# Kernel optimization log

Measured on AMD Instinct MI355X. Metric: run time of the kernel, lower is better.

The kernel has to match this reference:

```python
import jax, jax.numpy as jnp
import numpy as np

D_MODEL = 1024
HEADS = 16
D_HEAD = 64  # d_q = d_k = d_v
LN_EPS = 1e-5


def setup_inputs() -> dict:
    key = jax.random.key(0)
    ks = jax.random.split(key, 12)
    B, L = 2, 2048
    query = jax.random.normal(ks[0], (B, L, D_MODEL), dtype=jnp.float32)
    k_in = jax.random.normal(ks[1], (B, L, D_MODEL), dtype=jnp.float32)
    v_in = jax.random.normal(ks[2], (B, L, D_MODEL), dtype=jnp.float32)
    # causal mask: True = masked (masked_fill with -inf); row i always keeps pos i
    mask = jnp.broadcast_to(~jnp.tril(jnp.ones((L, L), dtype=bool)), (B, L, L))
    std_qk = np.sqrt(2.0 / (D_MODEL + D_HEAD)).astype(np.float32)
    Wq = jax.random.normal(ks[3], (D_MODEL, HEADS * D_HEAD), dtype=jnp.float32) * std_qk
    Wk = jax.random.normal(ks[4], (D_MODEL, HEADS * D_HEAD), dtype=jnp.float32) * std_qk
    Wv = jax.random.normal(ks[5], (D_MODEL, HEADS * D_HEAD), dtype=jnp.float32) * std_qk
    bq = jnp.zeros((HEADS * D_HEAD,), dtype=jnp.float32)
    bk = jnp.zeros((HEADS * D_HEAD,), dtype=jnp.float32)
    bv = jnp.zeros((HEADS * D_HEAD,), dtype=jnp.float32)
    lim = 1.0 / np.sqrt(HEADS * D_HEAD)
    Wo = jax.random.uniform(ks[6], (HEADS * D_HEAD, D_MODEL), dtype=jnp.float32, minval=-lim, maxval=lim)
    bo = jax.random.uniform(ks[7], (D_MODEL,), dtype=jnp.float32, minval=-lim, maxval=lim)
    gamma = jnp.ones((D_MODEL,), dtype=jnp.float32)
    beta = jnp.zeros((D_MODEL,), dtype=jnp.float32)
    return {"query": query, "key": k_in, "value": v_in, "mask": mask,
            "Wq": Wq, "bq": bq, "Wk": Wk, "bk": bk, "Wv": Wv, "bv": bv,
            "Wo": Wo, "bo": bo, "gamma": gamma, "beta": beta}


def reference(query, key, value, mask, Wq, bq, Wk, bk, Wv, bv, Wo, bo, gamma, beta):
    B, Lq, _ = query.shape
    Lk = key.shape[1]
    # QKV projections, split into heads: [B, L, H, d]
    q = (query @ Wq + bq).reshape(B, Lq, HEADS, D_HEAD)
    k = (key @ Wk + bk).reshape(B, Lk, HEADS, D_HEAD)
    v = (value @ Wv + bv).reshape(B, Lk, HEADS, D_HEAD)
    # scaled dot-product scores: [B, H, Lq, Lk]
    scores = jnp.einsum('bqhd,bkhd->bhqk', q, k) / np.sqrt(D_HEAD).astype(np.float32)
    scores = jnp.where(mask[:, None, :, :], -jnp.inf, scores)
    probs = jax.nn.softmax(scores, axis=-1)  # dropout is identity at p=0 / eval
    out = jnp.einsum('bhqk,bkhd->bqhd', probs, v).reshape(B, Lq, HEADS * D_HEAD)
    out = out @ Wo + bo  # dropout identity
    x = query + out  # residual
    mu = jnp.mean(x, axis=-1, keepdims=True)
    var = jnp.var(x, axis=-1, keepdims=True)
    return gamma * (x - mu) * jax.lax.rsqrt(var + LN_EPS) + beta
```

## Files before the change

### kernel.cpp

```cpp
#include <hip/hip_runtime.h>
#include <hip/hip_bf16.h>

#define L_SEQ  2048
#define DMODEL 1024
#define HEADS  16
#define DHEAD  64
#define BATCH  2
#define MROWS  (BATCH * L_SEQ)

typedef __attribute__((ext_vector_type(8))) short bf16x8;
typedef __attribute__((ext_vector_type(8))) unsigned short u16x8;
typedef __attribute__((ext_vector_type(4))) float f32x4;

__device__ __forceinline__ float b2f(unsigned short u) {
    union { unsigned int u32; float f; } x;
    x.u32 = ((unsigned int)u) << 16;
    return x.f;
}
__device__ __forceinline__ unsigned short f2b(float f) {
    union { float f; unsigned int u; } x; x.f = f;
    unsigned int u = x.u;
    if ((u & 0x7fffffffu) > 0x7f800000u) return (unsigned short)((u >> 16) | 0x0040);
    unsigned int r = (u + 0x7fffu + ((u >> 16) & 1u)) >> 16;
    return (unsigned short)r;
}
__device__ __forceinline__ unsigned short f2br(float f) {
    union { float f; unsigned int u; } x; x.f = f;
    return (unsigned short)((x.u + 0x7fffu + ((x.u >> 16) & 1u)) >> 16);
}

__device__ __forceinline__ float4 load4(const void* p, int isF32, size_t idx) {
    if (isF32) return *(const float4*)((const float*)p + idx);
    const ushort4 u = *(const ushort4*)((const unsigned short*)p + idx);
    return make_float4(b2f(u.x), b2f(u.y), b2f(u.z), b2f(u.w));
}
__device__ __forceinline__ float load1(const void* p, int isF32, size_t idx) {
    return isF32 ? ((const float*)p)[idx] : b2f(((const unsigned short*)p)[idx]);
}

__device__ __forceinline__ void gload16(const void* g, void* l) {
    __builtin_amdgcn_global_load_lds(
        (const __attribute__((address_space(1))) void*)g,
        (__attribute__((address_space(3))) void*)l, 16, 0, 0);
}

__global__ void detect_kernel(const unsigned short* __restrict__ q, int* __restrict__ flag) {
    int cnt = 0;
    #pragma unroll 8
    for (int t = 0; t < 64; ++t) {
        const unsigned short u = q[(threadIdx.x << 6) + t];
        const int e = (u >> 7) & 0xFF;
        cnt += (e >= 133) ? 1 : 0;
    }
    #pragma unroll
    for (int off = 32; off; off >>= 1) cnt += __shfl_xor(cnt, off);
    if (threadIdx.x == 0) *flag = (cnt > 64) ? 1 : 0;
}

__global__ void diag_kernel(float* __restrict__ out, float val, int n) {
    const int i = blockIdx.x * 256 + threadIdx.x;
    if (i < n) out[i] = val;
}

__global__ __launch_bounds__(256) void cvtW_kernel(
    const void* __restrict__ W0, const void* __restrict__ W1,
    const void* __restrict__ W2, const void* __restrict__ W3,
    unsigned short* __restrict__ T0, unsigned short* __restrict__ T1,
    unsigned short* __restrict__ T2, unsigned short* __restrict__ T3,
    const int* __restrict__ dflag)
{
    const int isF32 = *dflag;
    const int z = blockIdx.z;
    const void* W = (z == 0) ? W0 : (z == 1) ? W1 : (z == 2) ? W2 : W3;
    unsigned short* T = (z == 0) ? T0 : (z == 1) ? T1 : (z == 2) ? T2 : T3;

    __shared__ unsigned short tile[64][66];
    const int kb = blockIdx.x << 6, nb = blockIdx.y << 6;
    const int tr = threadIdx.x >> 4, tc = (threadIdx.x & 15) << 2;
    #pragma unroll
    for (int p = 0; p < 4; ++p) {
        const int r = tr + p * 16;
        const float4 v = load4(W, isF32, (size_t)(kb + r) * DMODEL + nb + tc);
        tile[tc + 0][r] = f2br(v.x);
        tile[tc + 1][r] = f2br(v.y);
        tile[tc + 2][r] = f2br(v.z);
        tile[tc + 3][r] = f2br(v.w);
    }
    __syncthreads();
    #pragma unroll
    for (int p = 0; p < 4; ++p) {
        const int rr = tr + p * 16;
        const ushort4 o = make_ushort4(tile[rr][tc], tile[rr][tc + 1],
                                       tile[rr][tc + 2], tile[rr][tc + 3]);
        *(ushort4*)(T + (size_t)(nb + rr) * DMODEL + kb + tc) = o;
    }
}

#define STAGE_B(BUF, K0)                                                          \
    gload16(Wt + (size_t)(colBase + bseg * 16 + brow) * DMODEL + (K0) + bcol,     \
            Bs[BUF] + bseg * 512);                                                \
    gload16(Wt + (size_t)(colBase + (bseg + 1) * 16 + brow) * DMODEL + (K0) + bcol,\
            Bs[BUF] + (bseg + 1) * 512);

#define QKV_COMPUTE(CUR)                                                          \
    {                                                                             \
        bf16x8 af[2], bfr[4];                                                     \
        _Pragma("unroll")                                                         \
        for (int i = 0; i < 2; ++i) {                                             \
            const int row = wm + i * 16 + ln;                                     \
            const int p = quad ^ ((row >> 1) & 3);                                \
            af[i] = *(const bf16x8*)(As[CUR] + row * 32 + p * 8);                 \
        }                                                                         \
        _Pragma("unroll")                                                         \
        for (int j = 0; j < 4; ++j)                                               \
            bfr[j] = *(const bf16x8*)(Bs[CUR] + (wn + j * 16 + ln) * 32 + quad * 8); \
        _Pragma("unroll")                                                         \
        for (int i = 0; i < 2; ++i)                                               \
            _Pragma("unroll")                                                     \
            for (int j = 0; j < 4; ++j)                                           \
                acc[i][j] = __builtin_amdgcn_mfma_f32_16x16x32_bf16(af[i], bfr[j], acc[i][j], 0, 0, 0); \
    }

__global__ __launch_bounds__(256) void gemm_qkv_mfma(
    const void* __restrict__ A0, const void* __restrict__ A1, const void* __restrict__ A2,
    const unsigned short* __restrict__ Wt0, const unsigned short* __restrict__ Wt1,
    const unsigned short* __restrict__ Wt2,
    const void* __restrict__ b0, const void* __restrict__ b1, const void* __restrict__ b2,
    unsigned short* __restrict__ O0, unsigned short* __restrict__ O1, unsigned short* __restrict__ O2,
    const int* __restrict__ dflag)
{
    const int isF32 = *dflag;

    const int bid = blockIdx.x;
    const int xcd = bid & 7;
    const int jj  = bid >> 3;
    const int g   = xcd * 24 + (jj >> 3);
    const int z   = g >> 6;
    const int rowBase = (g & 63) << 6;
    const int colBase = (jj & 7) << 7;

    const void* A  = (z == 0) ? A0 : (z == 1) ? A1 : A2;
    const unsigned short* Wt = (z == 0) ? Wt0 : (z == 1) ? Wt1 : Wt2;
    const void* bi = (z == 0) ? b0 : (z == 1) ? b1 : b2;
    unsigned short* out = (z == 0) ? O0 : (z == 1) ? O1 : O2;
    const float scale = (z == 0) ? 0.125f : 1.0f;

    __shared__ __align__(16) unsigned short As[2][64 * 32];
    __shared__ __align__(16) unsigned short Bs[2][128 * 32];

    const int tid  = threadIdx.x;
    const int lane = tid & 63, wid = tid >> 6;
    const int ln   = lane & 15, quad = lane >> 4;
    const int wm   = (wid & 1) << 5;
    const int wn   = (wid >> 1) << 6;

    f32x4 acc[2][4];
    #pragma unroll
    for (int i = 0; i < 2; ++i)
        #pragma unroll
        for (int j = 0; j < 4; ++j)
            #pragma unroll
            for (int d = 0; d < 4; ++d) acc[i][j][d] = 0.f;

    const int am  = tid >> 2;
    const int seg = tid & 3;
    const int sw  = (am >> 1) & 3;
    const int bseg = wid * 2;
    const int brow = lane >> 2, bcol = (lane & 3) << 3;

    if (isF32) {
        STAGE_B(0, 0)
        {
            const size_t ab = (size_t)(rowBase + am) * DMODEL + seg * 8;
            const float4 a0 = load4(A, 1, ab);
            const float4 a1 = load4(A, 1, ab + 4);
            u16x8 pk;
            pk[0] = f2br(a0.x); pk[1] = f2br(a0.y); pk[2] = f2br(a0.z); pk[3] = f2br(a0.w);
            pk[4] = f2br(a1.x); pk[5] = f2br(a1.y); pk[6] = f2br(a1.z); pk[7] = f2br(a1.w);
            *(u16x8*)(As[0] + am * 32 + ((seg ^ sw) << 3)) = pk;
        }
        __syncthreads();

        int cur = 0;
        for (int t = 0; t < 31; ++t) {
            const int nxt = cur ^ 1;
            const int k0n = (t + 1) << 5;
            STAGE_B(nxt, k0n)
            const size_t ab = (size_t)(rowBase + am) * DMODEL + k0n + seg * 8;
            const float4 a0 = load4(A, 1, ab);
            const float4 a1 = load4(A, 1, ab + 4);

            QKV_COMPUTE(cur)

            u16x8 pk;
            pk[0] = f2br(a0.x); pk[1] = f2br(a0.y); pk[2] = f2br(a0.z); pk[3] = f2br(a0.w);
            pk[4] = f2br(a1.x); pk[5] = f2br(a1.y); pk[6] = f2br(a1.z); pk[7] = f2br(a1.w);
            *(u16x8*)(As[nxt] + am * 32 + ((seg ^ sw) << 3)) = pk;

            __syncthreads();
            cur = nxt;
        }
        QKV_COMPUTE(cur)
    } else {
        const size_t asrc = (size_t)(rowBase + (tid >> 2)) * DMODEL +
                            (((tid & 3) ^ ((tid >> 3) & 3)) << 3);
        STAGE_B(0, 0)
        gload16((const unsigned short*)A + asrc, As[0] + wid * 512);
        __syncthreads();
        int cur = 0;
        for (int t = 0; t < 31; ++t) {
            const int nxt = cur ^ 1;
            const int k0n = (t + 1) << 5;
            STAGE_B(nxt, k0n)
            gload16((const unsigned short*)A + asrc + k0n, As[nxt] + wid * 512);
            QKV_COMPUTE(cur)
            __syncthreads();
            cur = nxt;
        }
        QKV_COMPUTE(cur)
    }

    float bsv[4];
    #pragma unroll
    for (int j = 0; j < 4; ++j) bsv[j] = load1(bi, isF32, colBase + wn + j * 16 + ln);

    if (z != 2) {
        #pragma unroll
        for (int i = 0; i < 2; ++i) {
            const int r0 = rowBase + wm + i * 16 + quad * 4;
            const int b = r0 >> 11, l0 = r0 & (L_SEQ - 1);
            #pragma unroll
            for (int j = 0; j < 4; ++j) {
                const int n = colBase + wn + j * 16 + ln;
                const int h = n >> 6, d = n & 63;
                const size_t base = ((size_t)(b * HEADS + h) * L_SEQ) << 6;
                #pragma unroll
                for (int reg = 0; reg < 4; ++reg)
                    out[base + ((size_t)(l0 + reg) << 6) + d] =
                        f2br((acc[i][j][reg] + bsv[j]) * scale);
            }
        }
    } else {
        #pragma unroll
        for (int i = 0; i < 2; ++i) {
            const int r0 = rowBase + wm + i * 16 + quad * 4;
            const int b = r0 >> 11, l0 = r0 & (L_SEQ - 1);
            #pragma unroll
            for (int j = 0; j < 4; ++j) {
                const int n = colBase + wn + j * 16 + ln;
                const int h = n >> 6, d = n & 63;
                ushort4 o;
                o.x = f2br(acc[i][j][0] + bsv[j]);
                o.y = f2br(acc[i][j][1] + bsv[j]);
                o.z = f2br(acc[i][j][2] + bsv[j]);
                o.w = f2br(acc[i][j][3] + bsv[j]);
                *(ushort4*)(out + (((size_t)((b * HEADS + h) * 64 + d)) << 11) + l0) = o;
            }
        }
    }
}

#define OSTAGE(BUF, K0)                                                           \
    gload16(AO + (size_t)(rowBase + wid * 16 + (lane >> 2)) * DMODEL + (K0) + ((lane & 3) << 3), \
            As[BUF] + wid * 512);                                                 \
    gload16(Wt + (size_t)(colBase + bseg * 16 + brow) * DMODEL + (K0) + bcol,     \
            Bs[BUF] + bseg * 512);                                                \
    gload16(Wt + (size_t)(colBase + (bseg + 1) * 16 + brow) * DMODEL + (K0) + bcol,\
            Bs[BUF] + (bseg + 1) * 512);

#define OUT_COMPUTE(CUR)                                                          \
    {                                                                             \
        bf16x8 af[2], bfr[4];                                                     \
        _Pragma("unroll")                                                         \
        for (int i = 0; i < 2; ++i)                                               \
            af[i] = *(const bf16x8*)(As[CUR] + (wm + i * 16 + ln) * 32 + quad * 8); \
        _Pragma("unroll")                                                         \
        for (int j = 0; j < 4; ++j)                                               \
            bfr[j] = *(const bf16x8*)(Bs[CUR] + (wn + j * 16 + ln) * 32 + quad * 8); \
        _Pragma("unroll")                                                         \
        for (int i = 0; i < 2; ++i)                                               \
            _Pragma("unroll")                                                     \
            for (int j = 0; j < 4; ++j)                                           \
                acc[i][j] = __builtin_amdgcn_mfma_f32_16x16x32_bf16(af[i], bfr[j], acc[i][j], 0, 0, 0); \
    }

__global__ __launch_bounds__(256) void gemm_out_mfma(
    const unsigned short* __restrict__ AO,
    const unsigned short* __restrict__ Wt,
    const void* __restrict__ bi,
    const void* __restrict__ resid,
    float* __restrict__ X,
    const int* __restrict__ dflag)
{
    const int isF32 = *dflag;
    __shared__ __align__(16) unsigned short As[2][64 * 32];
    __shared__ __align__(16) unsigned short Bs[2][128 * 32];

    const int bid = blockIdx.x;
    const int xcd = bid & 7;
    const int jj  = bid >> 3;
    const int g   = xcd * 8 + (jj >> 3);
    const int rowBase = g << 6;
    const int colBase = (jj & 7) << 7;

    const int tid  = threadIdx.x;
    const int lane = tid & 63, wid = tid >> 6;
    const int ln   = lane & 15, quad = lane >> 4;
    const int wm   = (wid & 1) << 5;
    const int wn   = (wid >> 1) << 6;

    f32x4 acc[2][4];
    #pragma unroll
    for (int i = 0; i < 2; ++i)
        #pragma unroll
        for (int j = 0; j < 4; ++j)
            #pragma unroll
            for (int d = 0; d < 4; ++d) acc[i][j][d] = 0.f;

    const int bseg = wid * 2;
    const int brow = lane >> 2, bcol = (lane & 3) << 3;

    OSTAGE(0, 0)
    __syncthreads();

    int cur = 0;
    for (int t = 0; t < 31; ++t) {
        const int nxt = cur ^ 1;
        const int k0n = (t + 1) << 5;
        OSTAGE(nxt, k0n)
        OUT_COMPUTE(cur)
        __syncthreads();
        cur = nxt;
    }
    OUT_COMPUTE(cur)

    float bsv[4];
    #pragma unroll
    for (int j = 0; j < 4; ++j) bsv[j] = load1(bi, isF32, colBase + wn + j * 16 + ln);

    #pragma unroll
    for (int i = 0; i < 2; ++i) {
        const int r0 = rowBase + wm + i * 16 + quad * 4;
        #pragma unroll
        for (int j = 0; j < 4; ++j) {
            const int n = colBase + wn + j * 16 + ln;
            #pragma unroll
            for (int reg = 0; reg < 4; ++reg) {
                const size_t idx = (size_t)(r0 + reg) * DMODEL + n;
                X[idx] = acc[i][j][reg] + bsv[j] + load1(resid, isF32, idx);
            }
        }
    }
}

#define KVB  128
#define NQB  (L_SEQ / 64)
#define KSTR 72
#define VSTR 136
__global__ __launch_bounds__(256, 3) void attn_mfma_kernel(
    const unsigned short* __restrict__ Q,
    const unsigned short* __restrict__ K,
    const unsigned short* __restrict__ Vt,
    unsigned short* __restrict__ AO)
{
    __shared__ unsigned short Kl[KVB * KSTR];
    __shared__ unsigned short Vl[64 * VSTR];
    __shared__ unsigned short Pl[4][16 * KVB];

    const int tid  = threadIdx.x;
    const int wid  = tid >> 6;
    const int lane = tid & 63;
    const int ln   = lane & 15;
    const int quad = lane >> 4;

    const int qb = (NQB - 1) - (blockIdx.x >> 5);
    const int bh = blockIdx.x & 31;

    const size_t qkBase = (size_t)bh * (L_SEQ * 64);
    const size_t vtBase = (size_t)bh * (64 * L_SEQ);

    const int qrow = qb * 64 + wid * 16 + ln;
    const bf16x8 qf0 = *(const bf16x8*)(Q + qkBase + (size_t)qrow * 64 + quad * 8);
    const bf16x8 qf1 = *(const bf16x8*)(Q + qkBase + (size_t)qrow * 64 + quad * 8 + 32);

    f32x4 o[4];
    #pragma unroll
    for (int d = 0; d < 4; ++d) { o[d][0] = 0.f; o[d][1] = 0.f; o[d][2] = 0.f; o[d][3] = 0.f; }
    float m[4] = {-INFINITY, -INFINITY, -INFINITY, -INFINITY};
    float l[4] = {0.f, 0.f, 0.f, 0.f};

    unsigned short* Pw = Pl[wid];
    const int kp_r = tid >> 3, kp_c = (tid & 7) * 8;
    const int vp_r = tid >> 4, vp_c = (tid & 15) * 8;

    const int nt = (qb >> 1) + 1;
    for (int jt = 0; jt < nt; ++jt) {
        __syncthreads();
        #pragma unroll
        for (int p = 0; p < 4; ++p) {
            const int kr = kp_r + p * 32;
            *(int4*)(Kl + kr * KSTR + kp_c) =
                *(const int4*)(K + qkBase + (size_t)(jt * KVB + kr) * 64 + kp_c);
            const int vr = vp_r + p * 16;
            *(int4*)(Vl + vr * VSTR + vp_c) =
                *(const int4*)(Vt + vtBase + (size_t)vr * L_SEQ + jt * KVB + vp_c);
        }
        __syncthreads();

        f32x4 s[8];
        __builtin_amdgcn_s_setprio(1);
        #pragma unroll
        for (int sub = 0; sub < 8; ++sub) {
            const bf16x8 kf0 = *(const bf16x8*)(Kl + (sub * 16 + ln) * KSTR + quad * 8);
            const bf16x8 kf1 = *(const bf16x8*)(Kl + (sub * 16 + ln) * KSTR + quad * 8 + 32);
            f32x4 a2;
            a2[0] = 0.f; a2[1] = 0.f; a2[2] = 0.f; a2[3] = 0.f;
            a2 = __builtin_amdgcn_mfma_f32_16x16x32_bf16(qf0, kf0, a2, 0, 0, 0);
            a2 = __builtin_amdgcn_mfma_f32_16x16x32_bf16(qf1, kf1, a2, 0, 0, 0);
            s[sub] = a2;
        }
        __builtin_amdgcn_s_setprio(0);

        if (jt == nt - 1) {
            const int row0 = qb * 64 + wid * 16 + quad * 4;
            #pragma unroll
            for (int sub = 0; sub < 8; ++sub) {
                const int keyg = jt * KVB + sub * 16 + ln;
                #pragma unroll
                for (int reg = 0; reg < 4; ++reg)
                    if (keyg > row0 + reg) s[sub][reg] = -INFINITY;
            }
        }

        float alpha[4];
        #pragma unroll
        for (int reg = 0; reg < 4; ++reg) {
            float t = fmaxf(
                fmaxf(fmaxf(s[0][reg], s[1][reg]), fmaxf(s[2][reg], s[3][reg])),
                fmaxf(fmaxf(s[4][reg], s[5][reg]), fmaxf(s[6][reg], s[7][reg])));
            #pragma unroll
            for (int off = 8; off; off >>= 1) t = fmaxf(t, __shfl_xor(t, off));
            const float mn = fmaxf(m[reg], t);
            alpha[reg] = __expf(m[reg] - mn);
            m[reg] = mn;
            float rs = 0.f;
            #pragma unroll
            for (int sub = 0; sub < 8; ++sub) {
                const float pe = __expf(s[sub][reg] - mn);
                s[sub][reg] = pe;
                rs += pe;
            }
            #pragma unroll
            for (int off = 8; off; off >>= 1) rs += __shfl_xor(rs, off);
            l[reg] = l[reg] * alpha[reg] + rs;
        }

        #pragma unroll
        for (int sub = 0; sub < 8; ++sub)
            #pragma unroll
            for (int reg = 0; reg < 4; ++reg) {
                const int r = quad * 4 + reg;
                const int blk = (sub * 2 + (ln >> 3)) ^ ((r >> 1) & 7);
                Pw[r * KVB + blk * 8 + (ln & 7)] = f2br(s[sub][reg]);
            }

        #pragma unroll
        for (int dblk = 0; dblk < 4; ++dblk)
            #pragma unroll
            for (int reg = 0; reg < 4; ++reg)
                o[dblk][reg] *= alpha[reg];

        __builtin_amdgcn_s_setprio(1);
        #pragma unroll
        for (int jb = 0; jb < 4; ++jb) {
            const int rblk = (jb * 4 + quad) ^ ((ln >> 1) & 7);
            const bf16x8 pf = *(const bf16x8*)(Pw + ln * KVB + rblk * 8);
            #pragma unroll
            for (int dblk = 0; dblk < 4; ++dblk) {
                const bf16x8 vf = *(const bf16x8*)(Vl + (dblk * 16 + ln) * VSTR + jb * 32 + quad * 8);
                o[dblk] = __builtin_amdgcn_mfma_f32_16x16x32_bf16(pf, vf, o[dblk], 0, 0, 0);
            }
        }
        __builtin_amdgcn_s_setprio(0);
    }

    const int b = bh >> 4, h = bh & 15;
    float rl[4];
    #pragma unroll
    for (int reg = 0; reg < 4; ++reg) rl[reg] = 1.f / l[reg];
    #pragma unroll
    for (int dblk = 0; dblk < 4; ++dblk)
        #pragma unroll
        for (int reg = 0; reg < 4; ++reg) {
            const int row = qb * 64 + wid * 16 + quad * 4 + reg;
            AO[((size_t)(b * L_SEQ + row)) * DMODEL + h * 64 + dblk * 16 + ln] =
                f2br(o[dblk][reg] * rl[reg]);
        }
}

__global__ __launch_bounds__(256) void ln_kernel(
    const float* __restrict__ X,
    const void* __restrict__ gamma,
    const void* __restrict__ beta,
    float* __restrict__ out,
    const int* __restrict__ dflag)
{
    const int isF32 = *dflag;
    const int row = blockIdx.x;
    const int tid = threadIdx.x;
    const float* x = X + (size_t)row * DMODEL;
    const int c0 = tid << 2;
    const float4 vv = *(const float4*)(x + c0);
    float s  = vv.x + vv.y + vv.z + vv.w;
    float s2 = vv.x * vv.x + vv.y * vv.y + vv.z * vv.z + vv.w * vv.w;
    #pragma unroll
    for (int off = 32; off; off >>= 1) {
        s  += __shfl_xor(s, off);
        s2 += __shfl_xor(s2, off);
    }
    __shared__ float red[4][2];
    const int wid = tid >> 6, lane = tid & 63;
    if (lane == 0) { red[wid][0] = s; red[wid][1] = s2; }
    __syncthreads();
    s  = red[0][0] + red[1][0] + red[2][0] + red[3][0];
    s2 = red[0][1] + red[1][1] + red[2][1] + red[3][1];
    const float mu  = s * (1.f / 1024.f);
    const float var = s2 * (1.f / 1024.f) - mu * mu;
    const float inv = rsqrtf(var + 1e-5f);
    const float4 gm = load4(gamma, isF32, c0);
    const float4 bt = load4(beta,  isF32, c0);
    float4 r;
    r.x = gm.x * (vv.x - mu) * inv + bt.x;
    r.y = gm.y * (vv.y - mu) * inv + bt.y;
    r.z = gm.z * (vv.z - mu) * inv + bt.z;
    r.w = gm.w * (vv.w - mu) * inv + bt.w;
    if (!(r.x == r.x) || fabsf(r.x) > 1e37f) r.x = 777000.0f;
    if (!(r.y == r.y) || fabsf(r.y) > 1e37f) r.y = 777000.0f;
    if (!(r.z == r.z) || fabsf(r.z) > 1e37f) r.z = 777000.0f;
    if (!(r.w == r.w) || fabsf(r.w) > 1e37f) r.w = 777000.0f;
    *(float4*)(out + (size_t)row * DMODEL + c0) = r;
}

extern "C" void kernel_launch(void* const* d_in, const int* in_sizes, int n_in,
                              void* d_out, int out_size, void* d_ws, size_t ws_size,
                              hipStream_t stream) {
    const void* query = d_in[0];
    const void* key   = d_in[1];
    const void* value = d_in[2];

    int wbase = 4;
    if (in_sizes[3] == DMODEL * DMODEL) wbase = 3;
    const void* Wq    = d_in[wbase + 0];
    const void* bq    = d_in[wbase + 1];
    const void* Wk    = d_in[wbase + 2];
    const void* bk    = d_in[wbase + 3];
    const void* Wv    = d_in[wbase + 4];
    const void* bv    = d_in[wbase + 5];
    const void* Wo    = d_in[wbase + 6];
    const void* bo    = d_in[wbase + 7];
    const void* gamma = d_in[wbase + 8];
    const void* beta  = d_in[wbase + 9];

    const size_t NEED = ((size_t)24u << 20) + 64;
    if (ws_size < NEED) {
        const float val = (float)(ws_size >> 20) * 1000.0f;
        diag_kernel<<<dim3((out_size + 255) / 256), dim3(256), 0, stream>>>(
            (float*)d_out, val, out_size);
        return;
    }

    char* ws = (char*)d_ws;
    unsigned short* Qb  = (unsigned short*)(ws);
    unsigned short* Kb  = (unsigned short*)(ws + (size_t)( 8u << 20));
    unsigned short* Vtb = (unsigned short*)(ws + (size_t)(16u << 20));
    float* X            = (float*)ws;
    int* dflag          = (int*)(ws + (size_t)(24u << 20));
    unsigned short* AO  = (unsigned short*)d_out;
    unsigned short* Wtq = (unsigned short*)d_out + ((size_t)4u << 20);
    unsigned short* Wtk = Wtq + ((size_t)1u << 20);
    unsigned short* Wtv = Wtk + ((size_t)1u << 20);
    unsigned short* Wto = Wtv + ((size_t)1u << 20);

    const dim3 blk(256);

    detect_kernel<<<dim3(1), dim3(64), 0, stream>>>((const unsigned short*)query, dflag);
    cvtW_kernel<<<dim3(16, 16, 4), blk, 0, stream>>>(
        Wq, Wk, Wv, Wo, Wtq, Wtk, Wtv, Wto, dflag);
    gemm_qkv_mfma<<<dim3(1536), blk, 0, stream>>>(
        query, key, value, Wtq, Wtk, Wtv, bq, bk, bv, Qb, Kb, Vtb, dflag);
    attn_mfma_kernel<<<dim3(BATCH * HEADS * 32), blk, 0, stream>>>(Qb, Kb, Vtb, AO);
    gemm_out_mfma<<<dim3(512), blk, 0, stream>>>(AO, Wto, bo, query, X, dflag);
    ln_kernel<<<dim3(MROWS), blk, 0, stream>>>(X, gamma, beta, (float*)d_out, dflag);
}
```

Before: 296.7 us.

## Triple-buffer B tiles and prefetch two K-steps ahead in QKV and output GEMMs

Both GEMMs now keep three LDS stages, so global loads for step t+2 are issued while step t is computed. In the QKV f32 path, only the weight tile gets a third buffer; the fp32 A prefetch is carried in registers one extra step ahead. The __syncthreads calls are replaced by explicit s_waitcnt (vmcnt(3) or lgkmcnt), s_barrier and sched_barrier, so outstanding loads are not drained at every step. This is meant to hide global-load latency better, at the cost of more LDS per block, which may reduce occupancy, and more fragile hand-written wait counts.

```diff
diff --git a/kernel.cpp b/kernel.cpp
--- a/kernel.cpp
+++ b/kernel.cpp
@@ -96,30 +96,34 @@
     }
 }
 
-#define STAGE_B(BUF, K0)                                                          \
+#define STAGE_B3(BP, K0)                                                          \
     gload16(Wt + (size_t)(colBase + bseg * 16 + brow) * DMODEL + (K0) + bcol,     \
-            Bs[BUF] + bseg * 512);                                                \
+            (BP) + bseg * 512);                                                   \
     gload16(Wt + (size_t)(colBase + (bseg + 1) * 16 + brow) * DMODEL + (K0) + bcol,\
-            Bs[BUF] + (bseg + 1) * 512);
-
-#define QKV_COMPUTE(CUR)                                                          \
+            (BP) + (bseg + 1) * 512);
+
+#define QKV_COMPUTE(AP, BP)                                                       \
     {                                                                             \
         bf16x8 af[2], bfr[4];                                                     \
         _Pragma("unroll")                                                         \
         for (int i = 0; i < 2; ++i) {                                             \
             const int row = wm + i * 16 + ln;                                     \
             const int p = quad ^ ((row >> 1) & 3);                                \
-            af[i] = *(const bf16x8*)(As[CUR] + row * 32 + p * 8);                 \
+            af[i] = *(const bf16x8*)((AP) + row * 32 + p * 8);                    \
         }                                                                         \
         _Pragma("unroll")                                                         \
         for (int j = 0; j < 4; ++j)                                               \
-            bfr[j] = *(const bf16x8*)(Bs[CUR] + (wn + j * 16 + ln) * 32 + quad * 8); \
+            bfr[j] = *(const bf16x8*)((BP) + (wn + j * 16 + ln) * 32 + quad * 8); \
         _Pragma("unroll")                                                         \
         for (int i = 0; i < 2; ++i)                                               \
             _Pragma("unroll")                                                     \
             for (int j = 0; j < 4; ++j)                                           \
                 acc[i][j] = __builtin_amdgcn_mfma_f32_16x16x32_bf16(af[i], bfr[j], acc[i][j], 0, 0, 0); \
     }
+
+#define PACK_A(PK, X0, X1)                                                        \
+    PK[0] = f2br(X0.x); PK[1] = f2br(X0.y); PK[2] = f2br(X0.z); PK[3] = f2br(X0.w); \
+    PK[4] = f2br(X1.x); PK[5] = f2br(X1.y); PK[6] = f2br(X1.z); PK[7] = f2br(X1.w);
 
 __global__ __launch_bounds__(256) void gemm_qkv_mfma(
     const void* __restrict__ A0, const void* __restrict__ A1, const void* __restrict__ A2,
@@ -146,7 +150,7 @@
     const float scale = (z == 0) ? 0.125f : 1.0f;
 
     __shared__ __align__(16) unsigned short As[2][64 * 32];
-    __shared__ __align__(16) unsigned short Bs[2][128 * 32];
+    __shared__ __align__(16) unsigned short Bs[3][128 * 32];
 
     const int tid  = threadIdx.x;
     const int lane = tid & 63, wid = tid >> 6;
@@ -169,55 +173,64 @@
     const int brow = lane >> 2, bcol = (lane & 3) << 3;
 
     if (isF32) {
-        STAGE_B(0, 0)
+        const size_t abase = (size_t)(rowBase + am) * DMODEL + seg * 8;
+        STAGE_B3(Bs[0], 0)
+        const float4 c0 = load4(A, 1, abase);
+        const float4 c1 = load4(A, 1, abase + 4);
+        STAGE_B3(Bs[1], 32)
+        float4 pA0 = load4(A, 1, abase + 32);
+        float4 pA1 = load4(A, 1, abase + 36);
         {
-            const size_t ab = (size_t)(rowBase + am) * DMODEL + seg * 8;
-            const float4 a0 = load4(A, 1, ab);
-            const float4 a1 = load4(A, 1, ab + 4);
             u16x8 pk;
-            pk[0] = f2br(a0.x); pk[1] = f2br(a0.y); pk[2] = f2br(a0.z); pk[3] = f2br(a0.w);
-            pk[4] = f2br(a1.x); pk[5] = f2br(a1.y); pk[6] = f2br(a1.z); pk[7] = f2br(a1.w);
+            PACK_A(pk, c0, c1)
             *(u16x8*)(As[0] + am * 32 + ((seg ^ sw) << 3)) = pk;
         }
-        __syncthreads();
-
-        int cur = 0;
+        asm volatile("s_waitcnt lgkmcnt(0)" ::: "memory");
+        __builtin_amdgcn_sched_barrier(0);
+        __builtin_amdgcn_s_barrier();
+        __builtin_amdgcn_sched_barrier(0);
+
         for (int t = 0; t < 31; ++t) {
-            const int nxt = cur ^ 1;
-            const int k0n = (t + 1) << 5;
-            STAGE_B(nxt, k0n)
-            const size_t ab = (size_t)(rowBase + am) * DMODEL + k0n + seg * 8;
-            const float4 a0 = load4(A, 1, ab);
-            const float4 a1 = load4(A, 1, ab + 4);
-
-            QKV_COMPUTE(cur)
-
-            u16x8 pk;
-            pk[0] = f2br(a0.x); pk[1] = f2br(a0.y); pk[2] = f2br(a0.z); pk[3] = f2br(a0.w);
-            pk[4] = f2br(a1.x); pk[5] = f2br(a1.y); pk[6] = f2br(a1.z); pk[7] = f2br(a1.w);
-            *(u16x8*)(As[nxt] + am * 32 + ((seg ^ sw) << 3)) = pk;
-
-            __syncthreads();
-            cur = nxt;
-        }
-        QKV_COMPUTE(cur)
+            float4 nA0, nA1;
+            if (t < 30) {
+                const int k2 = (t + 2) << 5;
+                STAGE_B3(Bs[(t + 2) % 3], k2)
+                nA0 = load4(A, 1, abase + k2);
+                nA1 = load4(A, 1, abase + k2 + 4);
+            }
+            __builtin_amdgcn_sched_barrier(0);
+
+            QKV_COMPUTE(As[t & 1], Bs[t % 3])
+
+            {
+                u16x8 pk;
+                PACK_A(pk, pA0, pA1)
+                *(u16x8*)(As[(t + 1) & 1] + am * 32 + ((seg ^ sw) << 3)) = pk;
+            }
+            if (t < 30) { pA0 = nA0; pA1 = nA1; }
+            asm volatile("s_waitcnt lgkmcnt(0)" ::: "memory");
+            __builtin_amdgcn_sched_barrier(0);
+            __builtin_amdgcn_s_barrier();
+            __builtin_amdgcn_sched_barrier(0);
+        }
+        QKV_COMPUTE(As[1], Bs[1])
     } else {
         const size_t asrc = (size_t)(rowBase + (tid >> 2)) * DMODEL +
                             (((tid & 3) ^ ((tid >> 3) & 3)) << 3);
-        STAGE_B(0, 0)
+        STAGE_B3(Bs[0], 0)
         gload16((const unsigned short*)A + asrc, As[0] + wid * 512);
         __syncthreads();
         int cur = 0;
         for (int t = 0; t < 31; ++t) {
             const int nxt = cur ^ 1;
             const int k0n = (t + 1) << 5;
-            STAGE_B(nxt, k0n)
+            STAGE_B3(Bs[nxt], k0n)
             gload16((const unsigned short*)A + asrc + k0n, As[nxt] + wid * 512);
-            QKV_COMPUTE(cur)
+            QKV_COMPUTE(As[cur], Bs[cur])
             __syncthreads();
             cur = nxt;
         }
-        QKV_COMPUTE(cur)
+        QKV_COMPUTE(As[cur], Bs[cur])
     }
 
     float bsv[4];
@@ -260,23 +273,23 @@
     }
 }
 
-#define OSTAGE(BUF, K0)                                                           \
+#define OSTAGE3(AP, BP, K0)                                                       \
     gload16(AO + (size_t)(rowBase + wid * 16 + (lane >> 2)) * DMODEL + (K0) + ((lane & 3) << 3), \
-            As[BUF] + wid * 512);                                                 \
+            (AP) + wid * 512);                                                    \
     gload16(Wt + (size_t)(colBase + bseg * 16 + brow) * DMODEL + (K0) + bcol,     \
-            Bs[BUF] + bseg * 512);                                                \
+            (BP) + bseg * 512);                                                   \
     gload16(Wt + (size_t)(colBase + (bseg + 1) * 16 + brow) * DMODEL + (K0) + bcol,\
-            Bs[BUF] + (bseg + 1) * 512);
-
-#define OUT_COMPUTE(CUR)                                                          \
+            (BP) + (bseg + 1) * 512);
+
+#define OUT_COMPUTE(AP, BP)                                                       \
     {                                                                             \
         bf16x8 af[2], bfr[4];                                                     \
         _Pragma("unroll")                                                         \
         for (int i = 0; i < 2; ++i)                                               \
-            af[i] = *(const bf16x8*)(As[CUR] + (wm + i * 16 + ln) * 32 + quad * 8); \
+            af[i] = *(const bf16x8*)((AP) + (wm + i * 16 + ln) * 32 + quad * 8);  \
         _Pragma("unroll")                                                         \
         for (int j = 0; j < 4; ++j)                                               \
-            bfr[j] = *(const bf16x8*)(Bs[CUR] + (wn + j * 16 + ln) * 32 + quad * 8); \
+            bfr[j] = *(const bf16x8*)((BP) + (wn + j * 16 + ln) * 32 + quad * 8); \
         _Pragma("unroll")                                                         \
         for (int i = 0; i < 2; ++i)                                               \
             _Pragma("unroll")                                                     \
@@ -293,8 +306,8 @@
     const int* __restrict__ dflag)
 {
     const int isF32 = *dflag;
-    __shared__ __align__(16) unsigned short As[2][64 * 32];
-    __shared__ __align__(16) unsigned short Bs[2][128 * 32];
+    __shared__ __align__(16) unsigned short As[3][64 * 32];
+    __shared__ __align__(16) unsigned short Bs[3][128 * 32];
 
     const int bid = blockIdx.x;
     const int xcd = bid & 7;
@@ -320,19 +333,26 @@
     const int bseg = wid * 2;
     const int brow = lane >> 2, bcol = (lane & 3) << 3;
 
-    OSTAGE(0, 0)
-    __syncthreads();
-
-    int cur = 0;
+    OSTAGE3(As[0], Bs[0], 0)
+    OSTAGE3(As[1], Bs[1], 32)
+    asm volatile("s_waitcnt vmcnt(3)" ::: "memory");
+    __builtin_amdgcn_sched_barrier(0);
+    __builtin_amdgcn_s_barrier();
+    __builtin_amdgcn_sched_barrier(0);
+
     for (int t = 0; t < 31; ++t) {
-        const int nxt = cur ^ 1;
-        const int k0n = (t + 1) << 5;
-        OSTAGE(nxt, k0n)
-        OUT_COMPUTE(cur)
-        __syncthreads();
-        cur = nxt;
-    }
-    OUT_COMPUTE(cur)
+        if (t < 30) { OSTAGE3(As[(t + 2) % 3], Bs[(t + 2) % 3], (t + 2) << 5) }
+        __builtin_amdgcn_sched_barrier(0);
+
+        OUT_COMPUTE(As[t % 3], Bs[t % 3])
+
+        if (t < 30) asm volatile("s_waitcnt vmcnt(3)" ::: "memory");
+        else        asm volatile("s_waitcnt vmcnt(0)" ::: "memory");
+        __builtin_amdgcn_sched_barrier(0);
+        __builtin_amdgcn_s_barrier();
+        __builtin_amdgcn_sched_barrier(0);
+    }
+    OUT_COMPUTE(As[1], Bs[1])
 
     float bsv[4];
     #pragma unroll
```

After: 293.2 us. Within noise of the previous version (-1.2%).

## Double K-depth of GEMM tiles and prefetch attention K/V into registers

Applied to the files above, without the earlier changes.

The QKV and output-projection GEMMs now stage 64-wide K slices instead of 32 into XOR-swizzled LDS, which halves the main-loop iterations and barriers and issues two MFMA k-chunks per stage. The attention kernel loads the next K/V tile into registers before computing on the current tile, then writes it to LDS afterwards, so global latency is hidden behind compute. The cost is double the LDS footprint in the GEMMs and extra registers in attention, which could lower occupancy under launch_bounds(256,3).

```diff
diff --git a/kernel.cpp b/kernel.cpp
--- a/kernel.cpp
+++ b/kernel.cpp
@@ -96,30 +96,50 @@
     }
 }
 
-#define STAGE_B(BUF, K0)                                                          \
-    gload16(Wt + (size_t)(colBase + bseg * 16 + brow) * DMODEL + (K0) + bcol,     \
-            Bs[BUF] + bseg * 512);                                                \
-    gload16(Wt + (size_t)(colBase + (bseg + 1) * 16 + brow) * DMODEL + (K0) + bcol,\
-            Bs[BUF] + (bseg + 1) * 512);
-
-#define QKV_COMPUTE(CUR)                                                          \
+#define STAGE_B64(BP, K0)                                                         \
+    _Pragma("unroll")                                                             \
+    for (int s = 0; s < 4; ++s)                                                   \
+        gload16(Wt + (size_t)(colBase + (wid << 5) + (s << 3) + brow8) * DMODEL + (K0) + bswz, \
+                (BP) + ((wid << 5) + (s << 3)) * 64);
+
+#define STAGE_A64(AP, BASE, K0)                                                   \
+    _Pragma("unroll")                                                             \
+    for (int s = 0; s < 2; ++s)                                                   \
+        gload16((BASE) + (size_t)(rowBase + (wid << 4) + (s << 3) + brow8) * DMODEL + (K0) + bswz, \
+                (AP) + ((wid << 4) + (s << 3)) * 64);
+
+#define GEMM_COMPUTE64(AP, BP)                                                    \
     {                                                                             \
-        bf16x8 af[2], bfr[4];                                                     \
+        bf16x8 af[2][2], bfr[4][2];                                               \
         _Pragma("unroll")                                                         \
         for (int i = 0; i < 2; ++i) {                                             \
             const int row = wm + i * 16 + ln;                                     \
-            const int p = quad ^ ((row >> 1) & 3);                                \
-            af[i] = *(const bf16x8*)(As[CUR] + row * 32 + p * 8);                 \
+            _Pragma("unroll")                                                     \
+            for (int kc = 0; kc < 2; ++kc)                                        \
+                af[i][kc] = *(const bf16x8*)((AP) + row * 64 +                    \
+                            ((((kc << 2) | quad) ^ (ln & 7)) << 3));              \
         }                                                                         \
         _Pragma("unroll")                                                         \
-        for (int j = 0; j < 4; ++j)                                               \
-            bfr[j] = *(const bf16x8*)(Bs[CUR] + (wn + j * 16 + ln) * 32 + quad * 8); \
+        for (int j = 0; j < 4; ++j) {                                             \
+            const int rowb = wn + j * 16 + ln;                                    \
+            _Pragma("unroll")                                                     \
+            for (int kc = 0; kc < 2; ++kc)                                        \
+                bfr[j][kc] = *(const bf16x8*)((BP) + rowb * 64 +                  \
+                            ((((kc << 2) | quad) ^ (ln & 7)) << 3));              \
+        }                                                                         \
         _Pragma("unroll")                                                         \
-        for (int i = 0; i < 2; ++i)                                               \
+        for (int kc = 0; kc < 2; ++kc)                                            \
             _Pragma("unroll")                                                     \
-            for (int j = 0; j < 4; ++j)                                           \
-                acc[i][j] = __builtin_amdgcn_mfma_f32_16x16x32_bf16(af[i], bfr[j], acc[i][j], 0, 0, 0); \
-    }
+            for (int i = 0; i < 2; ++i)                                           \
+                _Pragma("unroll")                                                 \
+                for (int j = 0; j < 4; ++j)                                       \
+                    acc[i][j] = __builtin_amdgcn_mfma_f32_16x16x32_bf16(          \
+                        af[i][kc], bfr[j][kc], acc[i][j], 0, 0, 0);               \
+    }
+
+#define PACK_A(PK, X0, X1)                                                        \
+    PK[0] = f2br(X0.x); PK[1] = f2br(X0.y); PK[2] = f2br(X0.z); PK[3] = f2br(X0.w); \
+    PK[4] = f2br(X1.x); PK[5] = f2br(X1.y); PK[6] = f2br(X1.z); PK[7] = f2br(X1.w);
 
 __global__ __launch_bounds__(256) void gemm_qkv_mfma(
     const void* __restrict__ A0, const void* __restrict__ A1, const void* __restrict__ A2,
@@ -145,8 +165,8 @@
     unsigned short* out = (z == 0) ? O0 : (z == 1) ? O1 : O2;
     const float scale = (z == 0) ? 0.125f : 1.0f;
 
-    __shared__ __align__(16) unsigned short As[2][64 * 32];
-    __shared__ __align__(16) unsigned short Bs[2][128 * 32];
+    __shared__ __align__(16) unsigned short As[2][64 * 64];
+    __shared__ __align__(16) unsigned short Bs[2][128 * 64];
 
     const int tid  = threadIdx.x;
     const int lane = tid & 63, wid = tid >> 6;
@@ -162,62 +182,65 @@
             #pragma unroll
             for (int d = 0; d < 4; ++d) acc[i][j][d] = 0.f;
 
-    const int am  = tid >> 2;
-    const int seg = tid & 3;
-    const int sw  = (am >> 1) & 3;
-    const int bseg = wid * 2;
-    const int brow = lane >> 2, bcol = (lane & 3) << 3;
+    const int brow8 = lane >> 3;
+    const int bswz  = ((lane & 7) ^ ((lane >> 3) & 7)) << 3;
 
     if (isF32) {
-        STAGE_B(0, 0)
+        const int am = tid >> 2, kseg = tid & 3;
+        const int c0 = (kseg << 1) ^ (am & 7), c1 = ((kseg << 1) | 1) ^ (am & 7);
+        const size_t abase = (size_t)(rowBase + am) * DMODEL + (kseg << 4);
+
+        STAGE_B64(Bs[0], 0)
         {
-            const size_t ab = (size_t)(rowBase + am) * DMODEL + seg * 8;
-            const float4 a0 = load4(A, 1, ab);
-            const float4 a1 = load4(A, 1, ab + 4);
-            u16x8 pk;
-            pk[0] = f2br(a0.x); pk[1] = f2br(a0.y); pk[2] = f2br(a0.z); pk[3] = f2br(a0.w);
-            pk[4] = f2br(a1.x); pk[5] = f2br(a1.y); pk[6] = f2br(a1.z); pk[7] = f2br(a1.w);
-            *(u16x8*)(As[0] + am * 32 + ((seg ^ sw) << 3)) = pk;
+            const float4 a0 = load4(A, 1, abase);
+            const float4 a1 = load4(A, 1, abase + 4);
+            const float4 a2 = load4(A, 1, abase + 8);
+            const float4 a3 = load4(A, 1, abase + 12);
+            u16x8 pk0, pk1;
+            PACK_A(pk0, a0, a1)
+            PACK_A(pk1, a2, a3)
+            *(u16x8*)(As[0] + am * 64 + (c0 << 3)) = pk0;
+            *(u16x8*)(As[0] + am * 64 + (c1 << 3)) = pk1;
         }
         __syncthreads();
 
         int cur = 0;
-        for (int t = 0; t < 31; ++t) {
+        for (int t = 0; t < 15; ++t) {
             const int nxt = cur ^ 1;
-            const int k0n = (t + 1) << 5;
-            STAGE_B(nxt, k0n)
-            const size_t ab = (size_t)(rowBase + am) * DMODEL + k0n + seg * 8;
-            const float4 a0 = load4(A, 1, ab);
-            const float4 a1 = load4(A, 1, ab + 4);
-
-            QKV_COMPUTE(cur)
-
-            u16x8 pk;
-            pk[0] = f2br(a0.x); pk[1] = f2br(a0.y); pk[2] = f2br(a0.z); pk[3] = f2br(a0.w);
-            pk[4] = f2br(a1.x); pk[5] = f2br(a1.y); pk[6] = f2br(a1.z); pk[7] = f2br(a1.w);
-            *(u16x8*)(As[nxt] + am * 32 + ((seg ^ sw) << 3)) = pk;
+            const int k0n = (t + 1) << 6;
+            STAGE_B64(Bs[nxt], k0n)
+            const float4 a0 = load4(A, 1, abase + k0n);
+            const float4 a1 = load4(A, 1, abase + k0n + 4);
+            const float4 a2 = load4(A, 1, abase + k0n + 8);
+            const float4 a3 = load4(A, 1, abase + k0n + 12);
+
+            GEMM_COMPUTE64(As[cur], Bs[cur])
+
+            u16x8 pk0, pk1;
+            PACK_A(pk0, a0, a1)
+            PACK_A(pk1, a2, a3)
+            *(u16x8*)(As[nxt] + am * 64 + (c0 << 3)) = pk0;
+            *(u16x8*)(As[nxt] + am * 64 + (c1 << 3)) = pk1;
 
             __syncthreads();
             cur = nxt;
         }
-        QKV_COMPUTE(cur)
+        GEMM_COMPUTE64(As[cur], Bs[cur])
     } else {
-        const size_t asrc = (size_t)(rowBase + (tid >> 2)) * DMODEL +
-                            (((tid & 3) ^ ((tid >> 3) & 3)) << 3);
-        STAGE_B(0, 0)
-        gload16((const unsigned short*)A + asrc, As[0] + wid * 512);
+        STAGE_B64(Bs[0], 0)
+        STAGE_A64(As[0], (const unsigned short*)A, 0)
         __syncthreads();
         int cur = 0;
-        for (int t = 0; t < 31; ++t) {
+        for (int t = 0; t < 15; ++t) {
             const int nxt = cur ^ 1;
-            const int k0n = (t + 1) << 5;
-            STAGE_B(nxt, k0n)
-            gload16((const unsigned short*)A + asrc + k0n, As[nxt] + wid * 512);
-            QKV_COMPUTE(cur)
+            const int k0n = (t + 1) << 6;
+            STAGE_B64(Bs[nxt], k0n)
+            STAGE_A64(As[nxt], (const unsigned short*)A, k0n)
+            GEMM_COMPUTE64(As[cur], Bs[cur])
             __syncthreads();
             cur = nxt;
         }
-        QKV_COMPUTE(cur)
+        GEMM_COMPUTE64(As[cur], Bs[cur])
     }
 
     float bsv[4];
@@ -260,30 +283,6 @@
     }
 }
 
-#define OSTAGE(BUF, K0)                                                           \
-    gload16(AO + (size_t)(rowBase + wid * 16 + (lane >> 2)) * DMODEL + (K0) + ((lane & 3) << 3), \
-            As[BUF] + wid * 512);                                                 \
-    gload16(Wt + (size_t)(colBase + bseg * 16 + brow) * DMODEL + (K0) + bcol,     \
-            Bs[BUF] + bseg * 512);                                                \
-    gload16(Wt + (size_t)(colBase + (bseg + 1) * 16 + brow) * DMODEL + (K0) + bcol,\
-            Bs[BUF] + (bseg + 1) * 512);
-
-#define OUT_COMPUTE(CUR)                                                          \
-    {                                                                             \
-        bf16x8 af[2], bfr[4];                                                     \
-        _Pragma("unroll")                                                         \
-        for (int i = 0; i < 2; ++i)                                               \
-            af[i] = *(const bf16x8*)(As[CUR] + (wm + i * 16 + ln) * 32 + quad * 8); \
-        _Pragma("unroll")                                                         \
-        for (int j = 0; j < 4; ++j)                                               \
-            bfr[j] = *(const bf16x8*)(Bs[CUR] + (wn + j * 16 + ln) * 32 + quad * 8); \
-        _Pragma("unroll")                                                         \
-        for (int i = 0; i < 2; ++i)                                               \
-            _Pragma("unroll")                                                     \
-            for (int j = 0; j < 4; ++j)                                           \
-                acc[i][j] = __builtin_amdgcn_mfma_f32_16x16x32_bf16(af[i], bfr[j], acc[i][j], 0, 0, 0); \
-    }
-
 __global__ __launch_bounds__(256) void gemm_out_mfma(
     const unsigned short* __restrict__ AO,
     const unsigned short* __restrict__ Wt,
@@ -293,8 +292,8 @@
     const int* __restrict__ dflag)
 {
     const int isF32 = *dflag;
-    __shared__ __align__(16) unsigned short As[2][64 * 32];
-    __shared__ __align__(16) unsigned short Bs[2][128 * 32];
+    __shared__ __align__(16) unsigned short As[2][64 * 64];
+    __shared__ __align__(16) unsigned short Bs[2][128 * 64];
 
     const int bid = blockIdx.x;
     const int xcd = bid & 7;
@@ -317,22 +316,24 @@
             #pragma unroll
             for (int d = 0; d < 4; ++d) acc[i][j][d] = 0.f;
 
-    const int bseg = wid * 2;
-    const int brow = lane >> 2, bcol = (lane & 3) << 3;
-
-    OSTAGE(0, 0)
+    const int brow8 = lane >> 3;
+    const int bswz  = ((lane & 7) ^ ((lane >> 3) & 7)) << 3;
+
+    STAGE_B64(Bs[0], 0)
+    STAGE_A64(As[0], AO, 0)
     __syncthreads();
 
     int cur = 0;
-    for (int t = 0; t < 31; ++t) {
+    for (int t = 0; t < 15; ++t) {
         const int nxt = cur ^ 1;
-        const int k0n = (t + 1) << 5;
-        OSTAGE(nxt, k0n)
-        OUT_COMPUTE(cur)
+        const int k0n = (t + 1) << 6;
+        STAGE_B64(Bs[nxt], k0n)
+        STAGE_A64(As[nxt], AO, k0n)
+        GEMM_COMPUTE64(As[cur], Bs[cur])
         __syncthreads();
         cur = nxt;
     }
-    OUT_COMPUTE(cur)
+    GEMM_COMPUTE64(As[cur], Bs[cur])
 
     float bsv[4];
     #pragma unroll
@@ -357,6 +358,20 @@
 #define NQB  (L_SEQ / 64)
 #define KSTR 72
 #define VSTR 136
+
+#define ALOAD(JT)                                                                 \
+    _Pragma("unroll")                                                             \
+    for (int p = 0; p < 4; ++p) {                                                 \
+        kreg[p] = *(const int4*)(K + qkBase + (size_t)((JT) * KVB + kp_r + p * 32) * 64 + kp_c); \
+        vreg[p] = *(const int4*)(Vt + vtBase + (size_t)(vp_r + p * 16) * L_SEQ + (JT) * KVB + vp_c); \
+    }
+#define AWRITE                                                                    \
+    _Pragma("unroll")                                                             \
+    for (int p = 0; p < 4; ++p) {                                                 \
+        *(int4*)(Kl + (kp_r + p * 32) * KSTR + kp_c) = kreg[p];                   \
+        *(int4*)(Vl + (vp_r + p * 16) * VSTR + vp_c) = vreg[p];                   \
+    }
+
 __global__ __launch_bounds__(256, 3) void attn_mfma_kernel(
     const unsigned short* __restrict__ Q,
     const unsigned short* __restrict__ K,
@@ -393,19 +408,15 @@
     const int kp_r = tid >> 3, kp_c = (tid & 7) * 8;
     const int vp_r = tid >> 4, vp_c = (tid & 15) * 8;
 
+    int4 kreg[4], vreg[4];
     const int nt = (qb >> 1) + 1;
+
+    ALOAD(0)
+    AWRITE
+    __syncthreads();
+
     for (int jt = 0; jt < nt; ++jt) {
-        __syncthreads();
-        #pragma unroll
-        for (int p = 0; p < 4; ++p) {
-            const int kr = kp_r + p * 32;
-            *(int4*)(Kl + kr * KSTR + kp_c) =
-                *(const int4*)(K + qkBase + (size_t)(jt * KVB + kr) * 64 + kp_c);
-            const int vr = vp_r + p * 16;
-            *(int4*)(Vl + vr * VSTR + vp_c) =
-                *(const int4*)(Vt + vtBase + (size_t)vr * L_SEQ + jt * KVB + vp_c);
-        }
-        __syncthreads();
+        if (jt + 1 < nt) { ALOAD(jt + 1) }
 
         f32x4 s[8];
         __builtin_amdgcn_s_setprio(1);
@@ -482,6 +493,12 @@
             }
         }
         __builtin_amdgcn_s_setprio(0);
+
+        __syncthreads();
+        if (jt + 1 < nt) {
+            AWRITE
+            __syncthreads();
+        }
     }
 
     const int b = bh >> 4, h = bh & 15;
```

Result: slower. 327.9 us (+10.5%).
